# Performance work log

Hardware: AMD Instinct MI355X
Metric: run time of the kernel (lower is better)

Reference implementation:

```python
import jax, jax.numpy as jnp
import numpy as np

ALPHA = 1.5
N_ITER = 50
DIM = -1


def setup_inputs() -> dict:
    key = jax.random.key(0)
    X = jax.random.normal(key, (8, 2048, 4096), dtype=jnp.float32)
    return {"X": X}


def reference(X):
    d = X.shape[DIM]
    alpha = jnp.asarray(ALPHA, X.dtype)
    Xs = (alpha - 1) * X
    m = jnp.max(Xs, axis=DIM, keepdims=True)
    t_min = m - 1
    t_max = m - jnp.asarray(d ** (1 - ALPHA), X.dtype)
    diff = t_max - t_min
    p = 1.0 / (d - 1)  # NOTE: source uses 1/(shape[dim]-1), reproduced faithfully

    def zfun(t):
        u = jnp.maximum(Xs - t, 0)
        u_safe = jnp.where(u > 0, u, 1.0)  # avoid nan grads of pow at 0
        return jnp.where(u > 0, u_safe ** p, 0.0)

    def body(carry, _):
        t_min, diff, _ = carry
        diff = diff / 2
        t = t_min + diff
        Z = zfun(t)
        mask = (jnp.sum(Z, axis=DIM, keepdims=True) - 1) >= 0
        t_min = jnp.where(mask, t, t_min)
        return (t_min, diff, t), None

    (t_min, diff, t), _ = jax.lax.scan(body, (t_min, diff, t_min), None, length=N_ITER)
    Z = zfun(t)  # Z from the final iteration's threshold t
    return Z / jnp.sum(Z, axis=DIM, keepdims=True)
```

## Files before the change

kernel.cpp:

```cpp
#include <hip/hip_runtime.h>
#include <math.h>


static constexpr int D = 4096;
static constexpr int NT = 256;
static constexpr float P = (float)(1.0 / 4095.0);

__device__ __forceinline__ float pow_p(float u) {
#if __has_builtin(__builtin_amdgcn_exp2f) && __has_builtin(__builtin_amdgcn_logf)
    return __builtin_amdgcn_exp2f(P * __builtin_amdgcn_logf(u));
#else
    return exp2f(P * log2f(u));
#endif
}

__device__ __forceinline__ float wave_sum(float v) {
#pragma unroll
    for (int k = 32; k >= 1; k >>= 1) v += __shfl_xor(v, k, 64);
    return v;
}

__device__ __forceinline__ void top2_merge(float& hi, float& lo, float ohi, float olo) {
    float nhi = fmaxf(hi, ohi);
    float nlo = fmaxf(fminf(hi, ohi), fmaxf(lo, olo));
    hi = nhi; lo = nlo;
}

__global__ void __launch_bounds__(NT) entmax_bisect_kernel(
        const float* __restrict__ X, float* __restrict__ out) {
    __shared__ float s_hi[4], s_lo[4], s_sum[4];

    const int tid  = threadIdx.x;
    const int lane = tid & 63;
    const int wid  = tid >> 6;
    const size_t rowbase = (size_t)blockIdx.x * D;
    const float4* Xv = (const float4*)(X + rowbase);
    float4*       Ov = (float4*)(out + rowbase);

    float4 xs[4];
#pragma unroll
    for (int c = 0; c < 4; ++c) {
        float4 v = Xv[c * NT + tid];
        xs[c].x = 0.5f * v.x; xs[c].y = 0.5f * v.y;
        xs[c].z = 0.5f * v.z; xs[c].w = 0.5f * v.w;
    }

    float hi = -3.4e38f, lo = -3.4e38f;
#pragma unroll
    for (int c = 0; c < 4; ++c) {
        const float vv[4] = {xs[c].x, xs[c].y, xs[c].z, xs[c].w};
#pragma unroll
        for (int j = 0; j < 4; ++j) {
            float v = vv[j];
            if (v > hi) { lo = hi; hi = v; }
            else        { lo = fmaxf(lo, v); }
        }
    }
#pragma unroll
    for (int k = 32; k >= 1; k >>= 1) {
        float ohi = __shfl_xor(hi, k, 64);
        float olo = __shfl_xor(lo, k, 64);
        top2_merge(hi, lo, ohi, olo);
    }
    if (lane == 0) { s_hi[wid] = hi; s_lo[wid] = lo; }
    __syncthreads();
    float m = s_hi[0], s2 = s_lo[0];
#pragma unroll
    for (int w = 1; w < 4; ++w) top2_merge(m, s2, s_hi[w], s_lo[w]);

    float t_min = m - 1.0f;
    float diff  = (m - 0.015625f) - t_min;
    float t     = t_min;
#pragma unroll 1
    for (int it = 0; it < 50; ++it) {
        diff *= 0.5f;
        t = t_min + diff;
        if (t == t_min) break;
        if (t < s2) t_min = t;
    }

    float local = 0.0f;
#pragma unroll
    for (int c = 0; c < 4; ++c) {
        const float vv[4] = {xs[c].x, xs[c].y, xs[c].z, xs[c].w};
#pragma unroll
        for (int j = 0; j < 4; ++j) {
            float u = vv[j] - t;
            if (u > 0.0f) local += pow_p(u);
        }
    }
    local = wave_sum(local);
    if (lane == 0) s_sum[wid] = local;
    __syncthreads();
    const float rsum = 1.0f / (s_sum[0] + s_sum[1] + s_sum[2] + s_sum[3]);

#pragma unroll
    for (int c = 0; c < 4; ++c) {
        float4 o; float u;
        u = xs[c].x - t; o.x = (u > 0.0f) ? pow_p(u) * rsum : 0.0f;
        u = xs[c].y - t; o.y = (u > 0.0f) ? pow_p(u) * rsum : 0.0f;
        u = xs[c].z - t; o.z = (u > 0.0f) ? pow_p(u) * rsum : 0.0f;
        u = xs[c].w - t; o.w = (u > 0.0f) ? pow_p(u) * rsum : 0.0f;
        Ov[c * NT + tid] = o;
    }
}

extern "C" void kernel_launch(void* const* d_in, const int* in_sizes, int n_in,
                              void* d_out, int out_size, void* d_ws, size_t ws_size,
                              hipStream_t stream) {
    const float* X = (const float*)d_in[0];
    float* O = (float*)d_out;
    const int nrows = in_sizes[0] / D;
    hipLaunchKernelGGL(entmax_bisect_kernel, dim3(nrows), dim3(NT), 0, stream, X, O);
}
```

Baseline: 428.1 us.

## Process eight rows per block with register prefetch and LDS-only barriers

Each block now handles eight consecutive rows instead of one. It loads the next row into registers while it computes the current row's top-2, bisection, sum and output. The __syncthreads calls are replaced with an inline s_waitcnt lgkmcnt(0) + s_barrier, so the barriers no longer wait for outstanding global loads and stores. The intent is to overlap HBM traffic with compute and cut per-block launch overhead. The cost is more live registers for the prefetch buffer and 8x fewer blocks, which could lower occupancy or leave the tail unbalanced.

```diff
diff --git a/kernel.cpp b/kernel.cpp
--- a/kernel.cpp
+++ b/kernel.cpp
@@ -2,9 +2,10 @@
 #include <math.h>
 
 
-static constexpr int D = 4096;
-static constexpr int NT = 256;
-static constexpr float P = (float)(1.0 / 4095.0);
+static constexpr int D    = 4096;
+static constexpr int NT   = 256;
+static constexpr int ROWS = 8;
+static constexpr float P  = (float)(1.0 / 4095.0);
 
 __device__ __forceinline__ float pow_p(float u) {
 #if __has_builtin(__builtin_amdgcn_exp2f) && __has_builtin(__builtin_amdgcn_logf)
@@ -12,6 +13,10 @@
 #else
     return exp2f(P * log2f(u));
 #endif
+}
+
+__device__ __forceinline__ void barrier_lds_only() {
+    __asm__ volatile("s_waitcnt lgkmcnt(0)\n\ts_barrier" ::: "memory");
 }
 
 __device__ __forceinline__ float wave_sum(float v) {
@@ -27,81 +32,100 @@
 }
 
 __global__ void __launch_bounds__(NT) entmax_bisect_kernel(
-        const float* __restrict__ X, float* __restrict__ out) {
+        const float* __restrict__ X, float* __restrict__ out, int nrows) {
     __shared__ float s_hi[4], s_lo[4], s_sum[4];
 
     const int tid  = threadIdx.x;
     const int lane = tid & 63;
     const int wid  = tid >> 6;
-    const size_t rowbase = (size_t)blockIdx.x * D;
-    const float4* Xv = (const float4*)(X + rowbase);
-    float4*       Ov = (float4*)(out + rowbase);
+    const int row0 = blockIdx.x * ROWS;
+    const int rows_here = min(ROWS, nrows - row0);
 
-    float4 xs[4];
+    const float4* Xv = (const float4*)X   + (size_t)row0 * (D / 4);
+    float4*       Ov = (float4*)out       + (size_t)row0 * (D / 4);
+
+    float4 cur[4], nxt[4];
 #pragma unroll
-    for (int c = 0; c < 4; ++c) {
-        float4 v = Xv[c * NT + tid];
-        xs[c].x = 0.5f * v.x; xs[c].y = 0.5f * v.y;
-        xs[c].z = 0.5f * v.z; xs[c].w = 0.5f * v.w;
-    }
-
-    float hi = -3.4e38f, lo = -3.4e38f;
-#pragma unroll
-    for (int c = 0; c < 4; ++c) {
-        const float vv[4] = {xs[c].x, xs[c].y, xs[c].z, xs[c].w};
-#pragma unroll
-        for (int j = 0; j < 4; ++j) {
-            float v = vv[j];
-            if (v > hi) { lo = hi; hi = v; }
-            else        { lo = fmaxf(lo, v); }
-        }
-    }
-#pragma unroll
-    for (int k = 32; k >= 1; k >>= 1) {
-        float ohi = __shfl_xor(hi, k, 64);
-        float olo = __shfl_xor(lo, k, 64);
-        top2_merge(hi, lo, ohi, olo);
-    }
-    if (lane == 0) { s_hi[wid] = hi; s_lo[wid] = lo; }
-    __syncthreads();
-    float m = s_hi[0], s2 = s_lo[0];
-#pragma unroll
-    for (int w = 1; w < 4; ++w) top2_merge(m, s2, s_hi[w], s_lo[w]);
-
-    float t_min = m - 1.0f;
-    float diff  = (m - 0.015625f) - t_min;
-    float t     = t_min;
-#pragma unroll 1
-    for (int it = 0; it < 50; ++it) {
-        diff *= 0.5f;
-        t = t_min + diff;
-        if (t == t_min) break;
-        if (t < s2) t_min = t;
-    }
-
-    float local = 0.0f;
-#pragma unroll
-    for (int c = 0; c < 4; ++c) {
-        const float vv[4] = {xs[c].x, xs[c].y, xs[c].z, xs[c].w};
-#pragma unroll
-        for (int j = 0; j < 4; ++j) {
-            float u = vv[j] - t;
-            if (u > 0.0f) local += pow_p(u);
-        }
-    }
-    local = wave_sum(local);
-    if (lane == 0) s_sum[wid] = local;
-    __syncthreads();
-    const float rsum = 1.0f / (s_sum[0] + s_sum[1] + s_sum[2] + s_sum[3]);
+    for (int c = 0; c < 4; ++c) cur[c] = Xv[c * NT + tid];
 
 #pragma unroll
-    for (int c = 0; c < 4; ++c) {
-        float4 o; float u;
-        u = xs[c].x - t; o.x = (u > 0.0f) ? pow_p(u) * rsum : 0.0f;
-        u = xs[c].y - t; o.y = (u > 0.0f) ? pow_p(u) * rsum : 0.0f;
-        u = xs[c].z - t; o.z = (u > 0.0f) ? pow_p(u) * rsum : 0.0f;
-        u = xs[c].w - t; o.w = (u > 0.0f) ? pow_p(u) * rsum : 0.0f;
-        Ov[c * NT + tid] = o;
+    for (int r = 0; r < ROWS; ++r) {
+        if (r >= rows_here) break;
+        if (r + 1 < rows_here) {
+            const float4* Xn = Xv + (size_t)(r + 1) * (D / 4);
+#pragma unroll
+            for (int c = 0; c < 4; ++c) nxt[c] = Xn[c * NT + tid];
+        }
+
+        float4 xs[4];
+#pragma unroll
+        for (int c = 0; c < 4; ++c) {
+            xs[c].x = 0.5f * cur[c].x; xs[c].y = 0.5f * cur[c].y;
+            xs[c].z = 0.5f * cur[c].z; xs[c].w = 0.5f * cur[c].w;
+        }
+
+        float hi = -3.4e38f, lo = -3.4e38f;
+#pragma unroll
+        for (int c = 0; c < 4; ++c) {
+            const float vv[4] = {xs[c].x, xs[c].y, xs[c].z, xs[c].w};
+#pragma unroll
+            for (int j = 0; j < 4; ++j) {
+                float v = vv[j];
+                if (v > hi) { lo = hi; hi = v; }
+                else        { lo = fmaxf(lo, v); }
+            }
+        }
+#pragma unroll
+        for (int k = 32; k >= 1; k >>= 1) {
+            float ohi = __shfl_xor(hi, k, 64);
+            float olo = __shfl_xor(lo, k, 64);
+            top2_merge(hi, lo, ohi, olo);
+        }
+        if (lane == 0) { s_hi[wid] = hi; s_lo[wid] = lo; }
+        barrier_lds_only();
+        float m = s_hi[0], s2 = s_lo[0];
+#pragma unroll
+        for (int w = 1; w < 4; ++w) top2_merge(m, s2, s_hi[w], s_lo[w]);
+
+        float t_min = m - 1.0f;
+        float diff  = (m - 0.015625f) - t_min;
+        float t     = t_min;
+#pragma unroll 1
+        for (int it = 0; it < 50; ++it) {
+            diff *= 0.5f;
+            t = t_min + diff;
+            if (t == t_min) break;
+            if (t < s2) t_min = t;
+        }
+
+        float local = 0.0f;
+#pragma unroll
+        for (int c = 0; c < 4; ++c) {
+            const float vv[4] = {xs[c].x, xs[c].y, xs[c].z, xs[c].w};
+#pragma unroll
+            for (int j = 0; j < 4; ++j) {
+                float u = vv[j] - t;
+                if (u > 0.0f) local += pow_p(u);
+            }
+        }
+        local = wave_sum(local);
+        if (lane == 0) s_sum[wid] = local;
+        barrier_lds_only();
+        const float rsum = 1.0f / (s_sum[0] + s_sum[1] + s_sum[2] + s_sum[3]);
+
+        float4* Or = Ov + (size_t)r * (D / 4);
+#pragma unroll
+        for (int c = 0; c < 4; ++c) {
+            float4 o; float u;
+            u = xs[c].x - t; o.x = (u > 0.0f) ? pow_p(u) * rsum : 0.0f;
+            u = xs[c].y - t; o.y = (u > 0.0f) ? pow_p(u) * rsum : 0.0f;
+            u = xs[c].z - t; o.z = (u > 0.0f) ? pow_p(u) * rsum : 0.0f;
+            u = xs[c].w - t; o.w = (u > 0.0f) ? pow_p(u) * rsum : 0.0f;
+            Or[c * NT + tid] = o;
+        }
+
+#pragma unroll
+        for (int c = 0; c < 4; ++c) cur[c] = nxt[c];
     }
 }
 
@@ -111,5 +135,7 @@
     const float* X = (const float*)d_in[0];
     float* O = (float*)d_out;
     const int nrows = in_sizes[0] / D;
-    hipLaunchKernelGGL(entmax_bisect_kernel, dim3(nrows), dim3(NT), 0, stream, X, O);
+    const int nblocks = (nrows + ROWS - 1) / ROWS;
+    hipLaunchKernelGGL(entmax_bisect_kernel, dim3(nblocks), dim3(NT), 0, stream,
+                       X, O, nrows);
 }
```

Result: slower. 440.9 us (+3.0%).
